# Performance work log

Hardware: AMD Instinct MI355X
Metric: run time of the kernel (lower is better)

Reference implementation:

```python
import jax, jax.numpy as jnp
import numpy as np
from jax import lax

B, DIM, L = 8, 512, 4096
GROUPS, NQ, CSIZE = 2, 8, 1024
DG = DIM // GROUPS


def setup_inputs() -> dict:
    key = jax.random.key(0)
    ks = jax.random.split(key, 10)
    s = 0.02
    return {
        "x": jax.random.normal(ks[0], (B, DIM, L), dtype=jnp.float32),
        "conv_enc_w": jax.random.normal(ks[1], (DIM, DIM, 3), dtype=jnp.float32) * s,
        "conv_enc_b": jnp.zeros((DIM,), jnp.float32),
        "pre_w": jax.random.normal(ks[2], (DIM, DIM), dtype=jnp.float32) * s,
        "pre_b": jnp.zeros((DIM,), jnp.float32),
        "codebooks": jax.random.normal(ks[3], (NQ, GROUPS, CSIZE, DG), dtype=jnp.float32) * s,
        "post_w": jax.random.normal(ks[4], (DIM, DIM), dtype=jnp.float32) * s,
        "post_b": jnp.zeros((DIM,), jnp.float32),
        "conv_dec_w": jax.random.normal(ks[5], (DIM, DIM, 3), dtype=jnp.float32) * s,
        "conv_dec_b": jnp.zeros((DIM,), jnp.float32),
    }


def _conv1d(x, w, b):
    # x: [b, d, l], w: [out, in, k], 'same' padding for k=3
    y = lax.conv_general_dilated(x, w, window_strides=(1,), padding=((1, 1),),
                                 dimension_numbers=("NCH", "OIH", "NCH"))
    return y + b[None, :, None]


def _grouped_residual_vq(h, codebooks):
    # h: [b, l, G, dg], codebooks: [Q, G, C, dg]
    b, l, g, dg = h.shape
    gidx = jnp.arange(g)[None, None, :]

    def step(carry, cb):
        residual, qout = carry
        # squared-euclidean argmin (||r||^2 term dropped: constant over codes)
        dots = jnp.einsum("blgd,gcd->blgc", residual, cb)
        c2 = jnp.sum(cb * cb, axis=-1)  # [g, c]
        idx = jnp.argmin(c2[None, None] - 2.0 * dots, axis=-1)  # [b, l, g]
        quant = cb[gidx, idx]  # gather -> [b, l, g, dg]
        commit = jnp.mean((residual - lax.stop_gradient(quant)) ** 2, axis=(0, 1, 3))  # [g]
        quant_st = residual + lax.stop_gradient(quant - residual)  # straight-through
        return (residual - lax.stop_gradient(quant), qout + quant_st), (idx, commit)

    (_, qout), (all_idx, all_loss) = lax.scan(step, (h, jnp.zeros_like(h)), codebooks)
    # all_idx: [Q, b, l, G] -> [G, b, l, Q]; all_loss: [Q, G] -> [G, Q]
    return qout, all_idx.transpose(3, 1, 2, 0), all_loss.T


def reference(x, conv_enc_w, conv_enc_b, pre_w, pre_b, codebooks,
              post_w, post_b, conv_dec_w, conv_dec_b):
    b, d, l = x.shape
    g = codebooks.shape[1]
    h = _conv1d(x, conv_enc_w, conv_enc_b)            # [b, d, l]
    h = h.transpose(0, 2, 1)                          # [b, l, d]
    h = h @ pre_w.T + pre_b                           # pre linear
    hg = h.reshape(b, l, g, d // g)                   # chunk dim into groups
    qout, indices, losses = _grouped_residual_vq(hg, codebooks)
    q = qout.reshape(b, l, d) @ post_w.T + post_b     # post linear
    q = q.transpose(0, 2, 1)                          # [b, d, l]
    _ = _conv1d(q, conv_dec_w, conv_dec_b)            # computed then discarded, as in original
    return (q, indices, losses)
```

## Files before the change

kernel.cpp:

```cpp
#include <hip/hip_runtime.h>
#include <cstdint>
#include <cstddef>

#define BB     8
#define DIMC   512
#define LL     4096
#define POSN   (BB*LL)
#define NG     2
#define NQ     8
#define CS     1024
#define DG     256

#define Q_OFF    0
#define IDX_OFF  16777216
#define LOSS_OFF 17301504

#define OFF_WFT   0
#define OFF_BF    786432
#define OFF_C2    786944
#define OFF_QH    803328
#define OFF_CANDD 17580544
#define OFF_CANDI 17842688
#define OFF_LOSSP 18104832
#define OFF_PWH   18121216

typedef _Float16 f16;
typedef _Float16 f16x8 __attribute__((ext_vector_type(8)));
typedef _Float16 f16x4 __attribute__((ext_vector_type(4)));
typedef float f32x4 __attribute__((ext_vector_type(4)));

#define LO_SCALE      1024.f
#define LO_INV        (1.f/1024.f)
#define F16_MIN_NORM  6.103515625e-05f

struct f16pair { f16 h, l; };

__device__ __forceinline__ f16pair split1(float v) {
    f16 hv = (f16)v;
    float hf = (float)hv;
    if (__builtin_fabsf(hf) < F16_MIN_NORM) { hv = (f16)0.f; hf = 0.f; }
    f16pair p;
    p.h = hv;
    p.l = (f16)((v - hf) * LO_SCALE);
    return p;
}

__device__ __forceinline__ void gload16(const void* g, void* l) {
    __builtin_amdgcn_global_load_lds(
        (const __attribute__((address_space(1))) void*)g,
        (__attribute__((address_space(3))) void*)l, 16, 0, 0);
}

__global__ __launch_bounds__(256) void k_fuse_w(const float* __restrict__ cw,
                                               const float* __restrict__ prew,
                                               float* __restrict__ wft) {
    __shared__ __align__(16) float As[16][68];
    __shared__ __align__(16) float Bs[16][68];
    int bid = blockIdx.x;
    int mt = bid >> 3, nt = bid & 7;
    int m0 = mt * 64, n0 = nt * 64;
    int t = threadIdx.x, tx = t & 15, ty = t >> 4;
    float acc[4][4] = {};
    for (int k0 = 0; k0 < 512; k0 += 16) {
        for (int u = t; u < 16 * 64; u += 256) {
            int kk = u >> 6, mm = u & 63;
            As[kk][mm] = cw[(size_t)(k0 + kk) * 1536 + m0 + mm];
        }
        {
            int r = t >> 2, c4 = t & 3;
            float4 v = *(const float4*)&prew[(size_t)(n0 + r) * 512 + k0 + c4 * 4];
            Bs[c4 * 4 + 0][r] = v.x; Bs[c4 * 4 + 1][r] = v.y;
            Bs[c4 * 4 + 2][r] = v.z; Bs[c4 * 4 + 3][r] = v.w;
        }
        __syncthreads();
#pragma unroll
        for (int k = 0; k < 16; ++k) {
            float4 a = *(const float4*)&As[k][ty * 4];
            float4 b = *(const float4*)&Bs[k][tx * 4];
            float av[4] = {a.x, a.y, a.z, a.w}, bv[4] = {b.x, b.y, b.z, b.w};
#pragma unroll
            for (int i = 0; i < 4; ++i)
#pragma unroll
                for (int j = 0; j < 4; ++j) acc[i][j] += av[i] * bv[j];
        }
        __syncthreads();
    }
#pragma unroll
    for (int i = 0; i < 4; ++i) {
        float4 v = {acc[i][0], acc[i][1], acc[i][2], acc[i][3]};
        *(float4*)&wft[(size_t)(m0 + ty * 4 + i) * 512 + n0 + tx * 4] = v;
    }
}

__global__ void k_bias(const float* __restrict__ prew, const float* __restrict__ preb,
                       const float* __restrict__ ceb, float* __restrict__ bf) {
    int dd = blockIdx.x * 256 + threadIdx.x;
    if (dd < 512) {
        float s = preb[dd];
        for (int j = 0; j < 512; ++j) s += prew[(size_t)dd * 512 + j] * ceb[j];
        bf[dd] = s;
    }
}

__global__ void k_c2(const float* __restrict__ cb, float* __restrict__ c2) {
    int wave = threadIdx.x >> 6, lane = threadIdx.x & 63;
    int row = blockIdx.x * 4 + wave;
    const float* r = cb + (size_t)row * 256;
    float4 v = *(const float4*)&r[lane * 4];
    float s = v.x * v.x + v.y * v.y + v.z * v.z + v.w * v.w;
#pragma unroll
    for (int m = 1; m < 64; m <<= 1) s += __shfl_xor(s, m);
    if (lane == 0) c2[row] = s;
}

__global__ void k_split_pw(const float* __restrict__ pw, f16* __restrict__ ph,
                           f16* __restrict__ pl) {
    size_t i = ((size_t)blockIdx.x * 256 + threadIdx.x) * 4;
    float4 v = *(const float4*)&pw[i];
    f16x4 hv, lv;
    f16pair p0 = split1(v.x), p1 = split1(v.y), p2 = split1(v.z), p3 = split1(v.w);
    hv.x = p0.h; lv.x = p0.l;
    hv.y = p1.h; lv.y = p1.l;
    hv.z = p2.h; lv.z = p2.l;
    hv.w = p3.h; lv.w = p3.l;
    *(f16x4*)&ph[i] = hv;
    *(f16x4*)&pl[i] = lv;
}

__global__ __launch_bounds__(256) void k_conv(const float* __restrict__ x,
                                              const float* __restrict__ wft,
                                              const float* __restrict__ bf,
                                              float* __restrict__ h) {
    int bid = blockIdx.x;
    int dt = bid >> 9;
    int rem = bid & 511;
    int bb = rem >> 6, lt = rem & 63;
    int l0 = lt * 64, d0 = dt * 64;
    int t = threadIdx.x, tx = t & 15, ty = t >> 4;
    __shared__ float Xs[8][68];
    __shared__ __align__(16) float Ws[24][64];
    float acc[4][4] = {};
    const float* xb = x + (size_t)bb * 512 * 4096;
    for (int i0 = 0; i0 < 512; i0 += 8) {
        for (int u = t; u < 8 * 66; u += 256) {
            int ii = u / 66, c = u % 66;
            int gl = l0 + c - 1;
            Xs[ii][c] = (gl >= 0 && gl < 4096) ? xb[(size_t)(i0 + ii) * 4096 + gl] : 0.f;
        }
        for (int u = t; u < 24 * 64; u += 256) {
            int r = u >> 6, c = u & 63;
            Ws[r][c] = wft[(size_t)(i0 * 3 + r) * 512 + d0 + c];
        }
        __syncthreads();
#pragma unroll
        for (int ii = 0; ii < 8; ++ii) {
            float a[6];
#pragma unroll
            for (int j = 0; j < 6; ++j) a[j] = Xs[ii][ty * 4 + j];
#pragma unroll
            for (int k = 0; k < 3; ++k) {
                float4 b = *(const float4*)&Ws[ii * 3 + k][tx * 4];
                float bv[4] = {b.x, b.y, b.z, b.w};
#pragma unroll
                for (int jl = 0; jl < 4; ++jl)
#pragma unroll
                    for (int jd = 0; jd < 4; ++jd) acc[jl][jd] += a[jl + k] * bv[jd];
            }
        }
        __syncthreads();
    }
    int posb = bb * 4096 + l0 + ty * 4;
    const float4 bias = *(const float4*)&bf[d0 + tx * 4];
#pragma unroll
    for (int jl = 0; jl < 4; ++jl) {
        float4 v = {acc[jl][0] + bias.x, acc[jl][1] + bias.y,
                    acc[jl][2] + bias.z, acc[jl][3] + bias.w};
        *(float4*)&h[(size_t)(posb + jl) * 512 + d0 + tx * 4] = v;
    }
}

__global__ __launch_bounds__(256) void k_dots(const float* __restrict__ hres,
                                              const float* __restrict__ cb,
                                              const float* __restrict__ c2,
                                              float* __restrict__ candd,
                                              int* __restrict__ candi,
                                              int q, int g) {
    __shared__ __align__(16) float As[16][132];
    __shared__ __align__(16) float Bs[16][132];
    __shared__ float Dd[16][128];
    __shared__ int   Di[16][128];
    int bid = blockIdx.x;
    int mt = bid >> 3, nt = bid & 7;
    int p0 = mt * 128, n0 = nt * 128;
    int t = threadIdx.x, pt = t & 15, ct = t >> 4;
    const float* cbq = cb + (size_t)(q * 2 + g) * 1024 * 256;
    const float* c2q = c2 + (q * 2 + g) * 1024;
    float acc[8][8] = {};
    for (int k0 = 0; k0 < 256; k0 += 16) {
        for (int u = t; u < 128 * 4; u += 256) {
            int r = u >> 2, c4 = u & 3;
            float4 v = *(const float4*)&hres[(size_t)(p0 + r) * 512 + g * 256 + k0 + c4 * 4];
            As[c4 * 4 + 0][r] = v.x; As[c4 * 4 + 1][r] = v.y;
            As[c4 * 4 + 2][r] = v.z; As[c4 * 4 + 3][r] = v.w;
        }
        for (int u = t; u < 128 * 4; u += 256) {
            int r = u >> 2, c4 = u & 3;
            float4 v = *(const float4*)&cbq[(size_t)(n0 + r) * 256 + k0 + c4 * 4];
            Bs[c4 * 4 + 0][r] = v.x; Bs[c4 * 4 + 1][r] = v.y;
            Bs[c4 * 4 + 2][r] = v.z; Bs[c4 * 4 + 3][r] = v.w;
        }
        __syncthreads();
#pragma unroll
        for (int k = 0; k < 16; ++k) {
            float4 a0 = *(const float4*)&As[k][pt * 8];
            float4 a1 = *(const float4*)&As[k][pt * 8 + 4];
            float4 b0 = *(const float4*)&Bs[k][ct * 8];
            float4 b1 = *(const float4*)&Bs[k][ct * 8 + 4];
            float av[8] = {a0.x, a0.y, a0.z, a0.w, a1.x, a1.y, a1.z, a1.w};
            float bv[8] = {b0.x, b0.y, b0.z, b0.w, b1.x, b1.y, b1.z, b1.w};
#pragma unroll
            for (int i = 0; i < 8; ++i)
#pragma unroll
                for (int j = 0; j < 8; ++j) acc[i][j] += av[i] * bv[j];
        }
        __syncthreads();
    }
#pragma unroll
    for (int i = 0; i < 8; ++i) {
        float bd = 1e30f; int bi = 0x7fffffff;
#pragma unroll
        for (int j = 0; j < 8; ++j) {
            int c = n0 + ct * 8 + j;
            float d = c2q[c] - 2.f * acc[i][j];
            if (d < bd) { bd = d; bi = c; }
        }
        Dd[ct][pt * 8 + i] = bd;
        Di[ct][pt * 8 + i] = bi;
    }
    __syncthreads();
    if (t < 128) {
        float bd = Dd[0][t]; int bi = Di[0][t];
#pragma unroll
        for (int j = 1; j < 16; ++j) {
            float d = Dd[j][t]; int i2 = Di[j][t];
            if (d < bd || (d == bd && i2 < bi)) { bd = d; bi = i2; }
        }
        candd[(size_t)(p0 + t) * 8 + nt] = bd;
        candi[(size_t)(p0 + t) * 8 + nt] = bi;
    }
}

__global__ __launch_bounds__(256) void k_fin(float* __restrict__ hres,
                                             const float* __restrict__ cb,
                                             const float* __restrict__ candd,
                                             const int* __restrict__ candi,
                                             float* __restrict__ lossp,
                                             float* __restrict__ idx_out,
                                             int q, int g) {
    int t = threadIdx.x, wave = t >> 6, lane = t & 63;
    const float* cbq = cb + (size_t)(q * 2 + g) * 1024 * 256;
    float lsum = 0.f;
    int pbase = blockIdx.x * 32 + wave * 8;
    for (int i = 0; i < 8; ++i) {
        int pos = pbase + i;
        float bd; int bi;
        if (lane < 8) { bd = candd[(size_t)pos * 8 + lane]; bi = candi[(size_t)pos * 8 + lane]; }
        else          { bd = 1e30f; bi = 0x7fffffff; }
#pragma unroll
        for (int m = 1; m < 8; m <<= 1) {
            float d2 = __shfl_xor(bd, m);
            int   i2 = __shfl_xor(bi, m);
            if (d2 < bd || (d2 == bd && i2 < bi)) { bd = d2; bi = i2; }
        }
        int idx = __shfl(bi, 0);
        float4 cv = *(const float4*)&cbq[(size_t)idx * 256 + lane * 4];
        size_t ro = (size_t)pos * 512 + g * 256 + lane * 4;
        float4 rv = *(const float4*)&hres[ro];
        float4 rn = {rv.x - cv.x, rv.y - cv.y, rv.z - cv.z, rv.w - cv.w};
        *(float4*)&hres[ro] = rn;
        lsum += rn.x * rn.x + rn.y * rn.y + rn.z * rn.z + rn.w * rn.w;
        if (lane == 0)
            idx_out[(size_t)(g * 32768 + pos) * 8 + q] = (float)idx;
    }
#pragma unroll
    for (int m = 1; m < 64; m <<= 1) lsum += __shfl_xor(lsum, m);
    __shared__ float ls[4];
    if (lane == 0) ls[wave] = lsum;
    __syncthreads();
    if (t == 0) lossp[(size_t)(g * 8 + q) * 1024 + blockIdx.x] = ls[0] + ls[1] + ls[2] + ls[3];
}

__global__ __launch_bounds__(256) void k_qsum2(const float* __restrict__ idxf,
                                               const float* __restrict__ cb,
                                               f16* __restrict__ qh,
                                               f16* __restrict__ ql) {
    int t = threadIdx.x, w = t >> 6, lane = t & 63;
    int pair = blockIdx.x * 4 + w;
    int g = pair & 1, pos = pair >> 1;
    const float* ip = idxf + ((size_t)g * 32768 + pos) * 8;
    float4 s = {0.f, 0.f, 0.f, 0.f};
    for (int qq = 0; qq < 8; ++qq) {
        int ii = (int)ip[qq];
        const float* rowp = cb + ((size_t)(qq * 2 + g) * 1024 + ii) * 256;
        float4 v = *(const float4*)&rowp[lane * 4];
        s.x += v.x; s.y += v.y; s.z += v.z; s.w += v.w;
    }
    f16x4 hv, lv;
    f16pair p0 = split1(s.x), p1 = split1(s.y), p2 = split1(s.z), p3 = split1(s.w);
    hv.x = p0.h; lv.x = p0.l;
    hv.y = p1.h; lv.y = p1.l;
    hv.z = p2.h; lv.z = p2.l;
    hv.w = p3.h; lv.w = p3.l;
    size_t o = (size_t)pos * 512 + g * 256 + lane * 4;
    *(f16x4*)&qh[o] = hv;
    *(f16x4*)&ql[o] = lv;
}

__global__ __launch_bounds__(256) void k_post_mfma(const f16* __restrict__ qh,
                                                   const f16* __restrict__ ql,
                                                   const f16* __restrict__ pwh,
                                                   const f16* __restrict__ pwl,
                                                   const float* __restrict__ pb,
                                                   float* __restrict__ out) {
    __shared__ __align__(16) f16 Ah[4096], Al[4096], Bh[4096], Bl[4096];
    int bid = blockIdx.x;
    int mt = bid >> 2, nt = bid & 3;
    int p0 = mt << 7, d0 = nt << 7;
    int t = threadIdx.x, w = t >> 6, lane = t & 63;
    int wm = (w >> 1) * 64, wn = (w & 1) * 64;
    const f16* gA;
    f16* lA;
    {
        const f16* a0 = qh + (size_t)p0 * 512;
        const f16* a1 = ql + (size_t)p0 * 512;
        const f16* b0 = pwh + (size_t)d0 * 512;
        const f16* b1 = pwl + (size_t)d0 * 512;
        gA = (w == 0) ? a0 : (w == 1) ? a1 : (w == 2) ? b0 : b1;
        lA = (w == 0) ? Ah : (w == 1) ? Al : (w == 2) ? Bh : Bl;
    }
    f32x4 acc[4][4] = {};
    f32x4 acc2[4][4] = {};
    int lr = lane & 15, kq = lane >> 4;
    for (int k0 = 0; k0 < 512; k0 += 32) {
#pragma unroll
        for (int u = 0; u < 8; ++u) {
            int kb = u >> 1, hf = u & 1;
            gload16(gA + (size_t)(hf * 64 + lane) * 512 + k0 + kb * 8,
                    lA + kb * 1024 + hf * 512);
        }
        __syncthreads();
        f16x8 a_h[4], a_l[4], b_h[4], b_l[4];
#pragma unroll
        for (int i = 0; i < 4; ++i) {
            int ao = kq * 1024 + (wm + i * 16 + lr) * 8;
            int bo = kq * 1024 + (wn + i * 16 + lr) * 8;
            a_h[i] = *(const f16x8*)&Ah[ao];
            a_l[i] = *(const f16x8*)&Al[ao];
            b_h[i] = *(const f16x8*)&Bh[bo];
            b_l[i] = *(const f16x8*)&Bl[bo];
        }
#pragma unroll
        for (int i = 0; i < 4; ++i)
#pragma unroll
            for (int j = 0; j < 4; ++j) {
                acc[i][j]  = __builtin_amdgcn_mfma_f32_16x16x32_f16(a_h[i], b_h[j], acc[i][j], 0, 0, 0);
                acc2[i][j] = __builtin_amdgcn_mfma_f32_16x16x32_f16(a_h[i], b_l[j], acc2[i][j], 0, 0, 0);
                acc2[i][j] = __builtin_amdgcn_mfma_f32_16x16x32_f16(a_l[i], b_h[j], acc2[i][j], 0, 0, 0);
            }
        __syncthreads();
    }
    int bb = p0 >> 12, l0 = p0 & 4095;
#pragma unroll
    for (int nj = 0; nj < 4; ++nj) {
        int dd = d0 + wn + nj * 16 + lr;
        float bias = pb[dd];
        float* orow = out + ((size_t)bb * 512 + dd) * 4096 + l0 + wm + kq * 4;
#pragma unroll
        for (int mi = 0; mi < 4; ++mi) {
            f32x4 v;
#pragma unroll
            for (int rg = 0; rg < 4; ++rg)
                v[rg] = acc[mi][nj][rg] + acc2[mi][nj][rg] * LO_INV + bias;
            *(f32x4*)&orow[mi * 16] = v;
        }
    }
}

__global__ void k_lossfin(const float* __restrict__ lossp, float* __restrict__ out) {
    int gq = blockIdx.x;
    float s = 0.f;
    for (int u = threadIdx.x; u < 1024; u += 256) s += lossp[(size_t)gq * 1024 + u];
    int wave = threadIdx.x >> 6, lane = threadIdx.x & 63;
#pragma unroll
    for (int m = 1; m < 64; m <<= 1) s += __shfl_xor(s, m);
    __shared__ float sh[4];
    if (lane == 0) sh[wave] = s;
    __syncthreads();
    if (threadIdx.x == 0)
        out[gq] = (sh[0] + sh[1] + sh[2] + sh[3]) * (1.f / (8.f * 4096.f * 256.f));
}

extern "C" void kernel_launch(void* const* d_in, const int* in_sizes, int n_in,
                              void* d_out, int out_size, void* d_ws, size_t ws_size,
                              hipStream_t stream) {
    (void)in_sizes; (void)n_in; (void)out_size; (void)ws_size;
    const float* x     = (const float*)d_in[0];
    const float* cew   = (const float*)d_in[1];
    const float* ceb   = (const float*)d_in[2];
    const float* prew  = (const float*)d_in[3];
    const float* preb  = (const float*)d_in[4];
    const float* cb    = (const float*)d_in[5];
    const float* postw = (const float*)d_in[6];
    const float* postb = (const float*)d_in[7];

    float* out = (float*)d_out;
    float* ws  = (float*)d_ws;
    float* wft   = ws + OFF_WFT;
    float* bf    = ws + OFF_BF;
    float* c2    = ws + OFF_C2;
    f16*   qh    = (f16*)(ws + OFF_QH);
    f16*   ql    = qh + 16777216;
    float* candd = ws + OFF_CANDD;
    int*   candi = (int*)(ws + OFF_CANDI);
    float* lossp = ws + OFF_LOSSP;
    f16*   pwh   = (f16*)(ws + OFF_PWH);
    f16*   pwl   = pwh + 262144;
    float* hres = out;

    k_fuse_w<<<192, 256, 0, stream>>>(cew, prew, wft);
    k_bias<<<2, 256, 0, stream>>>(prew, preb, ceb, bf);
    k_c2<<<4096, 256, 0, stream>>>(cb, c2);
    k_split_pw<<<256, 256, 0, stream>>>(postw, pwh, pwl);
    k_conv<<<4096, 256, 0, stream>>>(x, wft, bf, hres);
    for (int q = 0; q < 8; ++q) {
        for (int g = 0; g < 2; ++g) {
            k_dots<<<2048, 256, 0, stream>>>(hres, cb, c2, candd, candi, q, g);
            k_fin<<<1024, 256, 0, stream>>>(hres, cb, candd, candi, lossp,
                                            out + IDX_OFF, q, g);
        }
    }
    k_qsum2<<<16384, 256, 0, stream>>>(out + IDX_OFF, cb, qh, ql);
    k_post_mfma<<<1024, 256, 0, stream>>>(qh, ql, pwh, pwl, postb, out);
    k_lossfin<<<16, 256, 0, stream>>>(lossp, out + LOSS_OFF);
}
```

Before: 4.777 ms.

## Batch both VQ groups per launch and double-buffer k_dots shared tiles

Merges the two group launches of the distance and finalize kernels into single launches indexed by block id, with candidate buffers enlarged to hold both groups. This halves the number of launches in the residual-VQ loop and gives each launch more blocks. k_dots now prefetches the next K-slice into registers and double-buffers shared memory, dropping one barrier per iteration so global loads overlap the FMA work. Shared memory is reused for the reduction scratch, and the workspace offsets shift to fit the larger candidate arrays.

```diff
diff --git a/kernel.cpp b/kernel.cpp
--- a/kernel.cpp
+++ b/kernel.cpp
@@ -20,9 +20,9 @@
 #define OFF_C2    786944
 #define OFF_QH    803328
 #define OFF_CANDD 17580544
-#define OFF_CANDI 17842688
-#define OFF_LOSSP 18104832
-#define OFF_PWH   18121216
+#define OFF_CANDI 18104832
+#define OFF_LOSSP 18629120
+#define OFF_PWH   18645504
 
 typedef _Float16 f16;
 typedef _Float16 f16x8 __attribute__((ext_vector_type(8)));
@@ -184,38 +184,49 @@
                                               const float* __restrict__ c2,
                                               float* __restrict__ candd,
                                               int* __restrict__ candi,
-                                              int q, int g) {
-    __shared__ __align__(16) float As[16][132];
-    __shared__ __align__(16) float Bs[16][132];
-    __shared__ float Dd[16][128];
-    __shared__ int   Di[16][128];
+                                              int q) {
+    __shared__ __align__(16) float smem[8448];
     int bid = blockIdx.x;
-    int mt = bid >> 3, nt = bid & 7;
+    int g = bid >> 11;
+    int r = bid & 2047;
+    int mt = r >> 3, nt = r & 7;
     int p0 = mt * 128, n0 = nt * 128;
     int t = threadIdx.x, pt = t & 15, ct = t >> 4;
     const float* cbq = cb + (size_t)(q * 2 + g) * 1024 * 256;
     const float* c2q = c2 + (q * 2 + g) * 1024;
+    const float* pA = hres + (size_t)p0 * 512 + (size_t)g * 256;
+    const float* pB = cbq + (size_t)n0 * 256;
+    int r0 = t >> 2, c4 = t & 3;
+    int r1 = r0 + 64;
     float acc[8][8] = {};
-    for (int k0 = 0; k0 < 256; k0 += 16) {
-        for (int u = t; u < 128 * 4; u += 256) {
-            int r = u >> 2, c4 = u & 3;
-            float4 v = *(const float4*)&hres[(size_t)(p0 + r) * 512 + g * 256 + k0 + c4 * 4];
-            As[c4 * 4 + 0][r] = v.x; As[c4 * 4 + 1][r] = v.y;
-            As[c4 * 4 + 2][r] = v.z; As[c4 * 4 + 3][r] = v.w;
-        }
-        for (int u = t; u < 128 * 4; u += 256) {
-            int r = u >> 2, c4 = u & 3;
-            float4 v = *(const float4*)&cbq[(size_t)(n0 + r) * 256 + k0 + c4 * 4];
-            Bs[c4 * 4 + 0][r] = v.x; Bs[c4 * 4 + 1][r] = v.y;
-            Bs[c4 * 4 + 2][r] = v.z; Bs[c4 * 4 + 3][r] = v.w;
-        }
-        __syncthreads();
+    float4 va0 = *(const float4*)&pA[(size_t)r0 * 512 + c4 * 4];
+    float4 va1 = *(const float4*)&pA[(size_t)r1 * 512 + c4 * 4];
+    float4 vb0 = *(const float4*)&pB[(size_t)r0 * 256 + c4 * 4];
+    float4 vb1 = *(const float4*)&pB[(size_t)r1 * 256 + c4 * 4];
+    for (int c = 0; c < 16; ++c) {
+        int buf = c & 1;
+        float* wa = &smem[buf * 2112 + (c4 * 4) * 132];
+        float* wb = wa + 4224;
+        wa[r0] = va0.x; wa[132 + r0] = va0.y; wa[264 + r0] = va0.z; wa[396 + r0] = va0.w;
+        wa[r1] = va1.x; wa[132 + r1] = va1.y; wa[264 + r1] = va1.z; wa[396 + r1] = va1.w;
+        wb[r0] = vb0.x; wb[132 + r0] = vb0.y; wb[264 + r0] = vb0.z; wb[396 + r0] = vb0.w;
+        wb[r1] = vb1.x; wb[132 + r1] = vb1.y; wb[264 + r1] = vb1.z; wb[396 + r1] = vb1.w;
+        if (c < 15) {
+            int ko = (c + 1) * 16;
+            va0 = *(const float4*)&pA[(size_t)r0 * 512 + ko + c4 * 4];
+            va1 = *(const float4*)&pA[(size_t)r1 * 512 + ko + c4 * 4];
+            vb0 = *(const float4*)&pB[(size_t)r0 * 256 + ko + c4 * 4];
+            vb1 = *(const float4*)&pB[(size_t)r1 * 256 + ko + c4 * 4];
+        }
+        __syncthreads();
+        const float* Ab = &smem[buf * 2112];
+        const float* Bb = Ab + 4224;
 #pragma unroll
         for (int k = 0; k < 16; ++k) {
-            float4 a0 = *(const float4*)&As[k][pt * 8];
-            float4 a1 = *(const float4*)&As[k][pt * 8 + 4];
-            float4 b0 = *(const float4*)&Bs[k][ct * 8];
-            float4 b1 = *(const float4*)&Bs[k][ct * 8 + 4];
+            float4 a0 = *(const float4*)&Ab[k * 132 + pt * 8];
+            float4 a1 = *(const float4*)&Ab[k * 132 + pt * 8 + 4];
+            float4 b0 = *(const float4*)&Bb[k * 132 + ct * 8];
+            float4 b1 = *(const float4*)&Bb[k * 132 + ct * 8 + 4];
             float av[8] = {a0.x, a0.y, a0.z, a0.w, a1.x, a1.y, a1.z, a1.w};
             float bv[8] = {b0.x, b0.y, b0.z, b0.w, b1.x, b1.y, b1.z, b1.w};
 #pragma unroll
@@ -223,30 +234,31 @@
 #pragma unroll
                 for (int j = 0; j < 8; ++j) acc[i][j] += av[i] * bv[j];
         }
-        __syncthreads();
-    }
+    }
+    float* Dd = smem + 4224;
+    int*   Di = (int*)smem;
 #pragma unroll
     for (int i = 0; i < 8; ++i) {
         float bd = 1e30f; int bi = 0x7fffffff;
 #pragma unroll
         for (int j = 0; j < 8; ++j) {
-            int c = n0 + ct * 8 + j;
-            float d = c2q[c] - 2.f * acc[i][j];
-            if (d < bd) { bd = d; bi = c; }
-        }
-        Dd[ct][pt * 8 + i] = bd;
-        Di[ct][pt * 8 + i] = bi;
+            int cc = n0 + ct * 8 + j;
+            float d = c2q[cc] - 2.f * acc[i][j];
+            if (d < bd) { bd = d; bi = cc; }
+        }
+        Dd[ct * 128 + pt * 8 + i] = bd;
+        Di[ct * 128 + pt * 8 + i] = bi;
     }
     __syncthreads();
     if (t < 128) {
-        float bd = Dd[0][t]; int bi = Di[0][t];
+        float bd = Dd[t]; int bi = Di[t];
 #pragma unroll
         for (int j = 1; j < 16; ++j) {
-            float d = Dd[j][t]; int i2 = Di[j][t];
+            float d = Dd[j * 128 + t]; int i2 = Di[j * 128 + t];
             if (d < bd || (d == bd && i2 < bi)) { bd = d; bi = i2; }
         }
-        candd[(size_t)(p0 + t) * 8 + nt] = bd;
-        candi[(size_t)(p0 + t) * 8 + nt] = bi;
+        candd[((size_t)g * 32768 + p0 + t) * 8 + nt] = bd;
+        candi[((size_t)g * 32768 + p0 + t) * 8 + nt] = bi;
     }
 }
 
@@ -256,15 +268,17 @@
                                              const int* __restrict__ candi,
                                              float* __restrict__ lossp,
                                              float* __restrict__ idx_out,
-                                             int q, int g) {
+                                             int q) {
     int t = threadIdx.x, wave = t >> 6, lane = t & 63;
+    int g = blockIdx.x >> 10, blk = blockIdx.x & 1023;
     const float* cbq = cb + (size_t)(q * 2 + g) * 1024 * 256;
     float lsum = 0.f;
-    int pbase = blockIdx.x * 32 + wave * 8;
+    int pbase = blk * 32 + wave * 8;
     for (int i = 0; i < 8; ++i) {
         int pos = pbase + i;
+        size_t cbase = ((size_t)g * 32768 + pos) * 8;
         float bd; int bi;
-        if (lane < 8) { bd = candd[(size_t)pos * 8 + lane]; bi = candi[(size_t)pos * 8 + lane]; }
+        if (lane < 8) { bd = candd[cbase + lane]; bi = candi[cbase + lane]; }
         else          { bd = 1e30f; bi = 0x7fffffff; }
 #pragma unroll
         for (int m = 1; m < 8; m <<= 1) {
@@ -287,7 +301,7 @@
     __shared__ float ls[4];
     if (lane == 0) ls[wave] = lsum;
     __syncthreads();
-    if (t == 0) lossp[(size_t)(g * 8 + q) * 1024 + blockIdx.x] = ls[0] + ls[1] + ls[2] + ls[3];
+    if (t == 0) lossp[(size_t)(g * 8 + q) * 1024 + blk] = ls[0] + ls[1] + ls[2] + ls[3];
 }
 
 __global__ __launch_bounds__(256) void k_qsum2(const float* __restrict__ idxf,
@@ -433,11 +447,9 @@
     k_split_pw<<<256, 256, 0, stream>>>(postw, pwh, pwl);
     k_conv<<<4096, 256, 0, stream>>>(x, wft, bf, hres);
     for (int q = 0; q < 8; ++q) {
-        for (int g = 0; g < 2; ++g) {
-            k_dots<<<2048, 256, 0, stream>>>(hres, cb, c2, candd, candi, q, g);
-            k_fin<<<1024, 256, 0, stream>>>(hres, cb, candd, candi, lossp,
-                                            out + IDX_OFF, q, g);
-        }
+        k_dots<<<4096, 256, 0, stream>>>(hres, cb, c2, candd, candi, q);
+        k_fin<<<2048, 256, 0, stream>>>(hres, cb, candd, candi, lossp,
+                                        out + IDX_OFF, q);
     }
     k_qsum2<<<16384, 256, 0, stream>>>(out + IDX_OFF, cb, qh, ql);
     k_post_mfma<<<1024, 256, 0, stream>>>(qh, ql, pwh, pwl, postb, out);
```

After: 4.546 ms. 4.8% less time.
